# Performance work log

Measured on AMD Instinct MI355X. Metric: run time of the kernel, lower is better.

The kernel has to match this reference:

```python
import jax, jax.numpy as jnp
import numpy as np

N = 4096          # num_nodes == batch (every node sampled once)
D_EMB = 512       # n_embd (temporal encoder width)
D_GNN = 256       # gnn_embd
H = 2             # num_heads (hardcoded in GraphAttentionLayer default)
D_HEAD = D_GNN // H
FUS = D_EMB + D_GNN
EDGE_P = 32.0 / N # avg degree ~ max_neighbors
ALPHA = 0.2
NEG_INF = -9e15


def layer_norm(x, g, b, eps=1e-5):
    m = jnp.mean(x, axis=-1, keepdims=True)
    v = jnp.var(x, axis=-1, keepdims=True)
    return (x - m) / jnp.sqrt(v + eps) * g + b


def setup_inputs() -> dict:
    key = jax.random.key(0)
    ks = jax.random.split(key, 12)
    s = lambda fan: 1.0 / np.sqrt(fan)
    h_temporal = jax.random.normal(ks[0], (N, D_EMB), jnp.float32)
    node_indices = jnp.arange(N, dtype=jnp.int32)
    adj = (jax.random.uniform(ks[1], (N, N)) < EDGE_P).astype(jnp.float32)
    adj = jnp.maximum(adj, jnp.eye(N, dtype=jnp.float32))  # self-loops
    W_proj = jax.random.normal(ks[2], (D_EMB, D_GNN), jnp.float32) * s(D_EMB)
    b_proj = jnp.zeros((D_GNN,), jnp.float32)
    W_gat = jax.random.normal(ks[3], (H, D_GNN, D_HEAD), jnp.float32) * s(D_GNN)
    a_gat = jax.random.normal(ks[4], (H, 2 * D_HEAD), jnp.float32) * s(2 * D_HEAD)
    node_emb = jax.random.normal(ks[5], (N, D_GNN), jnp.float32) * 0.02
    ln_g = jnp.ones((D_GNN,), jnp.float32)
    ln_b = jnp.zeros((D_GNN,), jnp.float32)
    ln2_g = jnp.ones((FUS,), jnp.float32)
    ln2_b = jnp.zeros((FUS,), jnp.float32)
    W1 = jax.random.normal(ks[6], (FUS, FUS // 2), jnp.float32) * s(FUS)
    b1 = jnp.zeros((FUS // 2,), jnp.float32)
    W2 = jax.random.normal(ks[7], (FUS // 2, 1), jnp.float32) * s(FUS // 2)
    b2 = jnp.zeros((1,), jnp.float32)
    return dict(h_temporal=h_temporal, node_indices=node_indices, adj=adj,
                W_proj=W_proj, b_proj=b_proj, W_gat=W_gat, a_gat=a_gat,
                node_emb=node_emb, ln_g=ln_g, ln_b=ln_b,
                ln2_g=ln2_g, ln2_b=ln2_b, W1=W1, b1=b1, W2=W2, b2=b2)


def reference(h_temporal, node_indices, adj, W_proj, b_proj, W_gat, a_gat,
              node_emb, ln_g, ln_b, ln2_g, ln2_b, W1, b1, W2, b2):
    # gnn_proj
    h_gnn_in = h_temporal @ W_proj + b_proj                     # (B, D_GNN)
    # scatter-mean of batch features onto graph nodes (torch.unique + index_add_)
    counts = jax.ops.segment_sum(jnp.ones((h_gnn_in.shape[0],), h_gnn_in.dtype),
                                 node_indices, num_segments=N)
    sums = jax.ops.segment_sum(h_gnn_in, node_indices, num_segments=N)
    uniq_feats = sums / jnp.clip(counts, 1.0)[:, None]
    # nodes present in batch use averaged temporal feats, others keep learned embedding
    sub_feats = jnp.where((counts > 0)[:, None], uniq_feats, node_emb)  # (N, D_GNN)
    # multi-head GAT: e[h,i,j] = leakyrelu(a1_h . Wh_i + a2_h . Wh_j)
    Wh = jnp.einsum('ni,hid->hnd', sub_feats, W_gat)            # (H, N, d)
    f_src = jnp.einsum('hnd,hd->hn', Wh, a_gat[:, :D_HEAD])     # query half
    f_dst = jnp.einsum('hnd,hd->hn', Wh, a_gat[:, D_HEAD:])     # key half
    e = jax.nn.leaky_relu(f_src[:, :, None] + f_dst[:, None, :], ALPHA)  # (H,N,N)
    e = jnp.where(adj[None] > 0, e, NEG_INF)
    att = jax.nn.softmax(e, axis=-1)                            # softmax over neighbors j
    hp = jnp.einsum('hnm,hmd->hnd', att, Wh)                    # (H, N, d)
    hp = jnp.transpose(hp, (1, 0, 2)).reshape(N, D_GNN)         # concat heads
    hp = jax.nn.elu(hp)                                         # concat=True
    sub_out = layer_norm(hp, ln_g, ln_b)
    h_graph = sub_out[node_indices]                             # gather back to batch
    # fusion head
    hc = jnp.concatenate([h_temporal, h_graph], axis=-1)        # (B, FUS)
    z = layer_norm(hc, ln2_g, ln2_b)
    z = jax.nn.gelu(z @ W1 + b1, approximate=False)
    out = z @ W2 + b2                                           # (B, 1)
    return out
```

## Files before the change

### kernel.cpp

```cpp
#include <hip/hip_runtime.h>
#include <hip/hip_bf16.h>
#include <math.h>

#define N_NODES 4096
#define D_EMB   512
#define D_GNN   256
#define D_HEAD  128
#define FUS     768
#define D_HID   384
#define MAX_NBR 512

typedef unsigned short u16;
typedef __attribute__((ext_vector_type(4))) float f4;
typedef __attribute__((ext_vector_type(4))) int   i4;
typedef __attribute__((address_space(3))) u16 lds_u16;
typedef __attribute__((address_space(1))) const u16 g_u16;

__device__ __forceinline__ u16 bfh(float x) {
    __hip_bfloat16 b = __float2bfloat16(x);
    return *(u16*)&b;
}
__device__ __forceinline__ float bff(u16 u) {
    __hip_bfloat16 b = *(__hip_bfloat16*)&u;
    return __bfloat162float(b);
}

#define MFMA(acc, a, b) \
    asm volatile("v_mfma_f32_16x16x32_bf16 %0, %1, %2, %0" : "+v"(acc) : "v"(a), "v"(b))

__device__ __forceinline__ float block_reduce(float v, float* red, bool is_max) {
    #pragma unroll
    for (int o = 32; o; o >>= 1)
        v = is_max ? fmaxf(v, __shfl_down(v, o)) : v + __shfl_down(v, o);
    const int wid = threadIdx.x >> 6;
    if ((threadIdx.x & 63) == 0) red[wid] = v;
    __syncthreads();
    float r;
    if (is_max) r = fmaxf(fmaxf(red[0], red[1]), fmaxf(red[2], red[3]));
    else        r = red[0] + red[1] + red[2] + red[3];
    __syncthreads();
    return r;
}

__global__ __launch_bounds__(256) void split_rm(const float* __restrict__ X,
                                                u16* __restrict__ H, u16* __restrict__ L,
                                                int n4) {
    const int i = blockIdx.x * 256 + threadIdx.x;
    if (i >= n4) return;
    const float4 v = ((const float4*)X)[i];
    ushort4 h, l;
    h.x = bfh(v.x); l.x = bfh(v.x - bff(h.x));
    h.y = bfh(v.y); l.y = bfh(v.y - bff(h.y));
    h.z = bfh(v.z); l.z = bfh(v.z - bff(h.z));
    h.w = bfh(v.w); l.w = bfh(v.w - bff(h.w));
    ((ushort4*)H)[i] = h;
    ((ushort4*)L)[i] = l;
}

__global__ __launch_bounds__(256) void split_t(const float* __restrict__ W,
                                               u16* __restrict__ Th, u16* __restrict__ Tl,
                                               int K, int Nn) {
    __shared__ float tile[32][33];
    const int k0 = blockIdx.y * 32, n0 = blockIdx.x * 32;
    const int lx = threadIdx.x & 31, ly = threadIdx.x >> 5;
    #pragma unroll
    for (int r = ly; r < 32; r += 8)
        tile[r][lx] = W[(size_t)(k0 + r) * Nn + n0 + lx];
    __syncthreads();
    #pragma unroll
    for (int r = ly; r < 32; r += 8) {
        const float v = tile[lx][r];
        const u16 h = bfh(v);
        const size_t o = (size_t)(n0 + r) * K + k0 + lx;
        Th[o] = h;
        Tl[o] = bfh(v - bff(h));
    }
}

__global__ __launch_bounds__(256) void packbt(const float* __restrict__ Wgat,
                                              u16* __restrict__ Th, u16* __restrict__ Tl) {
    const int i = blockIdx.x;
    const int n = threadIdx.x;
    const int h = n >> 7, d = n & 127;
    const float v = Wgat[(size_t)h * D_GNN * D_HEAD + (size_t)i * D_HEAD + d];
    const u16 hh = bfh(v);
    Th[(size_t)n * D_GNN + i] = hh;
    Tl[(size_t)n * D_GNN + i] = bfh(v - bff(hh));
}

template<bool GELU, bool HASB>
__global__ __launch_bounds__(256) void mgemm(const u16* __restrict__ Ah, const u16* __restrict__ Al,
                                             const u16* __restrict__ Bh, const u16* __restrict__ Bl,
                                             const float* __restrict__ bias, float* __restrict__ C,
                                             int M, int Nn, int K) {
    __shared__ u16 lds[2][4][4096];
    const int t = threadIdx.x, w = t >> 6, l = t & 63;
    const int m0 = blockIdx.y * 64, n0 = blockIdx.x * 64;
    const int nk = K >> 6;
    const u16* pAh = Ah + (size_t)(m0 + (t >> 3)) * K + (t & 7) * 8;
    const u16* pAl = Al + (size_t)(m0 + (t >> 3)) * K + (t & 7) * 8;
    const u16* pBh = Bh + (size_t)(n0 + (t >> 3)) * K + (t & 7) * 8;
    const u16* pBl = Bl + (size_t)(n0 + (t >> 3)) * K + (t & 7) * 8;
    const int w512 = w * 512;
    const int K32 = K * 32;

#define STG(c, koff) do { \
    __builtin_amdgcn_global_load_lds((g_u16*)(pAh + (koff)),       (lds_u16*)&lds[c][0][w512],        16, 0, 0); \
    __builtin_amdgcn_global_load_lds((g_u16*)(pAh + (koff) + K32), (lds_u16*)&lds[c][0][w512 + 2048], 16, 0, 0); \
    __builtin_amdgcn_global_load_lds((g_u16*)(pAl + (koff)),       (lds_u16*)&lds[c][1][w512],        16, 0, 0); \
    __builtin_amdgcn_global_load_lds((g_u16*)(pAl + (koff) + K32), (lds_u16*)&lds[c][1][w512 + 2048], 16, 0, 0); \
    __builtin_amdgcn_global_load_lds((g_u16*)(pBh + (koff)),       (lds_u16*)&lds[c][2][w512],        16, 0, 0); \
    __builtin_amdgcn_global_load_lds((g_u16*)(pBh + (koff) + K32), (lds_u16*)&lds[c][2][w512 + 2048], 16, 0, 0); \
    __builtin_amdgcn_global_load_lds((g_u16*)(pBl + (koff)),       (lds_u16*)&lds[c][3][w512],        16, 0, 0); \
    __builtin_amdgcn_global_load_lds((g_u16*)(pBl + (koff) + K32), (lds_u16*)&lds[c][3][w512 + 2048], 16, 0, 0); \
} while (0)

    const int wm = w >> 1, wn = w & 1;
    const int lr = l & 15, lk = (l >> 4) << 3;
    int aoff[2][2], boff[2][2];
    #pragma unroll
    for (int i = 0; i < 2; ++i)
        #pragma unroll
        for (int ks = 0; ks < 2; ++ks) {
            aoff[i][ks] = (wm * 32 + i * 16 + lr) * 64 + ks * 32 + lk;
            boff[i][ks] = (wn * 32 + i * 16 + lr) * 64 + ks * 32 + lk;
        }

    f4 acc[2][2] = {};
    int cur = 0;
    STG(0, 0);
    __syncthreads();
    for (int kt = 0; kt < nk; ++kt) {
        if (kt + 1 < nk) STG(cur ^ 1, (kt + 1) * 64);
        const u16* LAh = lds[cur][0];
        const u16* LAl = lds[cur][1];
        const u16* LBh = lds[cur][2];
        const u16* LBl = lds[cur][3];
        i4 ah[2][2], al_[2][2], bh[2][2], bl_[2][2];
        #pragma unroll
        for (int i = 0; i < 2; ++i)
            #pragma unroll
            for (int ks = 0; ks < 2; ++ks) {
                ah[i][ks]  = *(const i4*)&LAh[aoff[i][ks]];
                al_[i][ks] = *(const i4*)&LAl[aoff[i][ks]];
                bh[i][ks]  = *(const i4*)&LBh[boff[i][ks]];
                bl_[i][ks] = *(const i4*)&LBl[boff[i][ks]];
            }
        #pragma unroll
        for (int i = 0; i < 2; ++i)
            #pragma unroll
            for (int j = 0; j < 2; ++j)
                #pragma unroll
                for (int ks = 0; ks < 2; ++ks) {
                    MFMA(acc[i][j], ah[i][ks],  bh[j][ks]);
                    MFMA(acc[i][j], ah[i][ks],  bl_[j][ks]);
                    MFMA(acc[i][j], al_[i][ks], bh[j][ks]);
                }
        __syncthreads();
        cur ^= 1;
    }
    asm volatile("s_nop 7\n\ts_nop 7\n\ts_nop 7");
    #pragma unroll
    for (int i = 0; i < 2; ++i)
        #pragma unroll
        for (int j = 0; j < 2; ++j) {
            const int col = n0 + wn * 32 + j * 16 + lr;
            float bv = 0.f;
            if (HASB) bv = bias[col];
            #pragma unroll
            for (int r = 0; r < 4; ++r) {
                const int row = m0 + wm * 32 + i * 16 + (l >> 4) * 4 + r;
                float v = acc[i][j][r] + bv;
                if (GELU) v = 0.5f * v * (1.f + erff(v * 0.70710678118654752f));
                C[(size_t)row * Nn + col] = v;
            }
        }
#undef STG
}

__global__ __launch_bounds__(256) void scatter_add(const float* __restrict__ hgnn,
                                                   const int* __restrict__ nidx,
                                                   float* __restrict__ sums,
                                                   float* __restrict__ counts) {
    const int b = blockIdx.x, t = threadIdx.x;
    const int g = nidx[b];
    atomicAdd(&sums[(size_t)g * D_GNN + t], hgnn[(size_t)b * D_GNN + t]);
    if (t == 0) atomicAdd(&counts[g], 1.0f);
}

__global__ __launch_bounds__(256) void combine(const float* __restrict__ sums,
                                               const float* __restrict__ counts,
                                               const float* __restrict__ nemb,
                                               u16* __restrict__ subh,
                                               u16* __restrict__ subl) {
    const int n = blockIdx.x, t = threadIdx.x;
    const float c = counts[n];
    const size_t o = (size_t)n * D_GNN + t;
    const float v = (c > 0.f) ? sums[o] / fmaxf(c, 1.f) : nemb[o];
    const u16 h = bfh(v);
    subh[o] = h;
    subl[o] = bfh(v - bff(h));
}

__global__ __launch_bounds__(256) void fsd(const float* __restrict__ Wh,
                                           const float* __restrict__ agat,
                                           float* __restrict__ fsrc,
                                           float* __restrict__ fdst) {
    const int n = blockIdx.x * 4 + (threadIdx.x >> 6);
    const int l = threadIdx.x & 63;
    const float* row = Wh + (size_t)n * D_GNN;
    const float x0 = row[l],       x1 = row[l + 64];
    const float y0 = row[128 + l], y1 = row[192 + l];
    float s0 = x0 * agat[l]       + x1 * agat[l + 64];
    float s1 = x0 * agat[128 + l] + x1 * agat[192 + l];
    float s2 = y0 * agat[256 + l] + y1 * agat[320 + l];
    float s3 = y0 * agat[384 + l] + y1 * agat[448 + l];
    #pragma unroll
    for (int o = 32; o; o >>= 1) {
        s0 += __shfl_down(s0, o); s1 += __shfl_down(s1, o);
        s2 += __shfl_down(s2, o); s3 += __shfl_down(s3, o);
    }
    if (l == 0) {
        fsrc[n] = s0;            fdst[n] = s1;
        fsrc[N_NODES + n] = s2;  fdst[N_NODES + n] = s3;
    }
}

__global__ __launch_bounds__(256) void gat_attn(const float* __restrict__ adj,
                                                const float* __restrict__ Wh,
                                                const float* __restrict__ fsrc,
                                                const float* __restrict__ fdst,
                                                const float* __restrict__ lng,
                                                const float* __restrict__ lnb,
                                                float* __restrict__ subout) {
    const int i = blockIdx.x, t = threadIdx.x;
    const int lane = t & 63, wid = t >> 6;
    __shared__ int   s_nbr[MAX_NBR];
    __shared__ int   s_wsum[4];
    __shared__ float s_att[2][MAX_NBR];
    __shared__ float s_red[4];
    __shared__ float s_inv[2];

    const float4* arow4 = (const float4*)(adj + (size_t)i * N_NODES) + t * 4;
    const float4 c0 = arow4[0], c1 = arow4[1], c2 = arow4[2], c3 = arow4[3];
    float v[16];
    *(float4*)&v[0]  = c0; *(float4*)&v[4]  = c1;
    *(float4*)&v[8]  = c2; *(float4*)&v[12] = c3;
    int mask = 0;
    #pragma unroll
    for (int k = 0; k < 16; ++k) mask |= (v[k] > 0.f) ? (1 << k) : 0;
    const int cnt_t = __popc(mask);

    int pre = cnt_t;
    #pragma unroll
    for (int o = 1; o < 64; o <<= 1) {
        const int u = __shfl_up(pre, o);
        if (lane >= o) pre += u;
    }
    if (lane == 63) s_wsum[wid] = pre;
    __syncthreads();
    int base = 0;
    for (int w = 0; w < wid; ++w) base += s_wsum[w];
    const int total = s_wsum[0] + s_wsum[1] + s_wsum[2] + s_wsum[3];
    int off = base + pre - cnt_t;
    #pragma unroll
    for (int k = 0; k < 16; ++k)
        if ((mask >> k) & 1) {
            if (off < MAX_NBR) s_nbr[off] = t * 16 + k;
            ++off;
        }
    __syncthreads();
    const int cnt = min(total, MAX_NBR);

    for (int h = 0; h < 2; ++h) {
        const float fs = fsrc[h * N_NODES + i];
        const float* fd = fdst + h * N_NODES;
        float lm = -1e30f;
        for (int idx = t; idx < cnt; idx += 256) {
            float e = fs + fd[s_nbr[idx]];
            e = e > 0.f ? e : 0.2f * e;
            s_att[h][idx] = e;
            lm = fmaxf(lm, e);
        }
        const float m = block_reduce(lm, s_red, true);
        float ls = 0.f;
        for (int idx = t; idx < cnt; idx += 256) {
            const float p = expf(s_att[h][idx] - m);
            s_att[h][idx] = p;
            ls += p;
        }
        const float s = block_reduce(ls, s_red, false);
        if (t == 0) s_inv[h] = 1.f / s;
    }
    __syncthreads();

    const int h = t >> 7, d = t & 127;
    float acc = 0.f;
    for (int j = 0; j < cnt; ++j)
        acc += s_att[h][j] * Wh[(size_t)s_nbr[j] * D_GNN + h * D_HEAD + d];
    acc *= s_inv[h];
    const float vv = acc > 0.f ? acc : expm1f(acc);
    const float sum  = block_reduce(vv, s_red, false);
    const float sq   = block_reduce(vv * vv, s_red, false);
    const float mean = sum * (1.f / 256.f);
    const float var  = sq * (1.f / 256.f) - mean * mean;
    const float rstd = rsqrtf(var + 1e-5f);
    subout[(size_t)i * D_GNN + t] = (vv - mean) * rstd * lng[t] + lnb[t];
}

__global__ __launch_bounds__(256) void fuse_ln(const float* __restrict__ ht,
                                               const float* __restrict__ subout,
                                               const int* __restrict__ nidx,
                                               const float* __restrict__ g,
                                               const float* __restrict__ b,
                                               u16* __restrict__ znh,
                                               u16* __restrict__ znl) {
    const int row = blockIdx.x, t = threadIdx.x;
    __shared__ float s_red[4];
    const int gidx = nidx[row];
    const float x0 = ht[(size_t)row * D_EMB + t];
    const float x1 = ht[(size_t)row * D_EMB + 256 + t];
    const float x2 = subout[(size_t)gidx * D_GNN + t];
    const float sum = block_reduce(x0 + x1 + x2, s_red, false);
    const float sq  = block_reduce(x0 * x0 + x1 * x1 + x2 * x2, s_red, false);
    const float mean = sum * (1.f / 768.f);
    const float var  = sq * (1.f / 768.f) - mean * mean;
    const float rstd = rsqrtf(var + 1e-5f);
    const size_t base = (size_t)row * FUS;
    const float z0 = (x0 - mean) * rstd * g[t]       + b[t];
    const float z1 = (x1 - mean) * rstd * g[256 + t] + b[256 + t];
    const float z2 = (x2 - mean) * rstd * g[512 + t] + b[512 + t];
    u16 h;
    h = bfh(z0); znh[base + t]       = h; znl[base + t]       = bfh(z0 - bff(h));
    h = bfh(z1); znh[base + 256 + t] = h; znl[base + 256 + t] = bfh(z1 - bff(h));
    h = bfh(z2); znh[base + 512 + t] = h; znl[base + 512 + t] = bfh(z2 - bff(h));
}

__global__ __launch_bounds__(256) void outk(const float* __restrict__ z1,
                                            const float* __restrict__ W2,
                                            const float* __restrict__ b2,
                                            float* __restrict__ out) {
    const int row = blockIdx.x * 4 + (threadIdx.x >> 6);
    const int l = threadIdx.x & 63;
    float acc = 0.f;
    for (int c = l; c < D_HID; c += 64)
        acc += z1[(size_t)row * D_HID + c] * W2[c];
    #pragma unroll
    for (int o = 32; o; o >>= 1) acc += __shfl_down(acc, o);
    if (l == 0) out[row] = acc + b2[0];
}

extern "C" void kernel_launch(void* const* d_in, const int* in_sizes, int n_in,
                              void* d_out, int out_size, void* d_ws, size_t ws_size,
                              hipStream_t stream) {
    const float* ht    = (const float*)d_in[0];
    const int*   nidx  = (const int*)  d_in[1];
    const float* adj   = (const float*)d_in[2];
    const float* Wproj = (const float*)d_in[3];
    const float* bproj = (const float*)d_in[4];
    const float* Wgat  = (const float*)d_in[5];
    const float* agat  = (const float*)d_in[6];
    const float* nemb  = (const float*)d_in[7];
    const float* lng   = (const float*)d_in[8];
    const float* lnb   = (const float*)d_in[9];
    const float* ln2g  = (const float*)d_in[10];
    const float* ln2b  = (const float*)d_in[11];
    const float* W1    = (const float*)d_in[12];
    const float* b1    = (const float*)d_in[13];
    const float* W2    = (const float*)d_in[14];
    const float* b2    = (const float*)d_in[15];
    float* out = (float*)d_out;

    const size_t MB = 1u << 20;
    char* base = (char*)d_ws;
    u16*   ht_hi  = (u16*)(base);
    u16*   ht_lo  = ht_hi + 2097152;
    u16*   zn_hi  = (u16*)(base);
    u16*   zn_lo  = zn_hi + 3145728;
    float* f_hgnn = (float*)(base + 12 * MB);
    float* f_z1   = (float*)(base + 12 * MB);
    float* f_sums = (float*)(base + 18 * MB);
    float* f_cnt  = (float*)(base + 22 * MB);
    u16*   subf_h = (u16*)(base + 22 * MB + 65536);
    u16*   subf_l = subf_h + 1048576;
    u16*   bT_h   = (u16*)(base + 27 * MB);
    u16*   bT_l   = bT_h + 65536;
    u16*   WpT_h  = (u16*)(base + 28 * MB);
    u16*   WpT_l  = WpT_h + 131072;
    float* f_wh   = (float*)(base + 29 * MB);
    float* f_fsrc = (float*)(base + 33 * MB);
    float* f_fdst = (float*)(base + 33 * MB + 32768);
    float* f_subo = (float*)(base + 34 * MB);
    u16*   W1T_h  = (u16*)(base + 38 * MB);
    u16*   W1T_l  = W1T_h + 294912;

    hipMemsetAsync(f_sums, 0, (1048576 + 4096) * sizeof(float), stream);

    split_rm<<<2048, 256, 0, stream>>>(ht, ht_hi, ht_lo, 524288);
    split_t<<<dim3(8, 16), 256, 0, stream>>>(Wproj, WpT_h, WpT_l, D_EMB, D_GNN);
    mgemm<false, true><<<dim3(4, 64), 256, 0, stream>>>(
        ht_hi, ht_lo, WpT_h, WpT_l, bproj, f_hgnn, N_NODES, D_GNN, D_EMB);
    scatter_add<<<N_NODES, 256, 0, stream>>>(f_hgnn, nidx, f_sums, f_cnt);
    combine<<<N_NODES, 256, 0, stream>>>(f_sums, f_cnt, nemb, subf_h, subf_l);
    packbt<<<D_GNN, 256, 0, stream>>>(Wgat, bT_h, bT_l);
    mgemm<false, false><<<dim3(4, 64), 256, 0, stream>>>(
        subf_h, subf_l, bT_h, bT_l, nullptr, f_wh, N_NODES, D_GNN, D_GNN);
    fsd<<<N_NODES / 4, 256, 0, stream>>>(f_wh, agat, f_fsrc, f_fdst);
    gat_attn<<<N_NODES, 256, 0, stream>>>(adj, f_wh, f_fsrc, f_fdst, lng, lnb, f_subo);
    fuse_ln<<<N_NODES, 256, 0, stream>>>(ht, f_subo, nidx, ln2g, ln2b, zn_hi, zn_lo);
    split_t<<<dim3(12, 24), 256, 0, stream>>>(W1, W1T_h, W1T_l, FUS, D_HID);
    mgemm<true, true><<<dim3(6, 64), 256, 0, stream>>>(
        zn_hi, zn_lo, W1T_h, W1T_l, b1, f_z1, N_NODES, D_HID, FUS);
    outk<<<N_NODES / 4, 256, 0, stream>>>(f_z1, W2, b2, out);
}
```

Baseline: 214.8 us.

## Split-K the three GEMMs with reduce kernels and merge weight prep launches

Each split-bf16 GEMM now runs with a K split of two across grid z, writing partial results to separate buffers. A new elementwise reduce kernel sums the two partials and applies bias and GELU. The three weight transpose and split kernels are merged into one launch, and the workspace layout is rebuilt without aliasing. The goal is to double the block count on GEMM grids of 256 to 384 blocks so more of the GPU's compute units stay busy. The cost is extra partial-result global traffic and two additional launches.

```diff
diff --git a/kernel.cpp b/kernel.cpp
--- a/kernel.cpp
+++ b/kernel.cpp
@@ -57,11 +57,11 @@
     ((ushort4*)L)[i] = l;
 }
 
-__global__ __launch_bounds__(256) void split_t(const float* __restrict__ W,
-                                               u16* __restrict__ Th, u16* __restrict__ Tl,
-                                               int K, int Nn) {
-    __shared__ float tile[32][33];
-    const int k0 = blockIdx.y * 32, n0 = blockIdx.x * 32;
+__device__ __forceinline__ void split_t_body(const float* __restrict__ W,
+                                             u16* __restrict__ Th, u16* __restrict__ Tl,
+                                             int K, int Nn, int bx, int by,
+                                             float (*tile)[33]) {
+    const int k0 = by * 32, n0 = bx * 32;
     const int lx = threadIdx.x & 31, ly = threadIdx.x >> 5;
     #pragma unroll
     for (int r = ly; r < 32; r += 8)
@@ -77,26 +77,41 @@
     }
 }
 
-__global__ __launch_bounds__(256) void packbt(const float* __restrict__ Wgat,
-                                              u16* __restrict__ Th, u16* __restrict__ Tl) {
-    const int i = blockIdx.x;
-    const int n = threadIdx.x;
-    const int h = n >> 7, d = n & 127;
-    const float v = Wgat[(size_t)h * D_GNN * D_HEAD + (size_t)i * D_HEAD + d];
-    const u16 hh = bfh(v);
-    Th[(size_t)n * D_GNN + i] = hh;
-    Tl[(size_t)n * D_GNN + i] = bfh(v - bff(hh));
-}
-
-template<bool GELU, bool HASB>
+__global__ __launch_bounds__(256) void prep_w(const float* __restrict__ Wproj,
+                                              const float* __restrict__ W1,
+                                              const float* __restrict__ Wgat,
+                                              u16* __restrict__ WpTh, u16* __restrict__ WpTl,
+                                              u16* __restrict__ W1Th, u16* __restrict__ W1Tl,
+                                              u16* __restrict__ bTh,  u16* __restrict__ bTl) {
+    __shared__ float tile[32][33];
+    const int b = blockIdx.x;
+    if (b < 128) {
+        split_t_body(Wproj, WpTh, WpTl, D_EMB, D_GNN, b & 7, b >> 3, tile);
+    } else if (b < 416) {
+        const int i = b - 128;
+        split_t_body(W1, W1Th, W1Tl, FUS, D_HID, i % 12, i / 12, tile);
+    } else {
+        const int i = b - 416;
+        const int n = threadIdx.x;
+        const int h = n >> 7, d = n & 127;
+        const float v = Wgat[(size_t)h * D_GNN * D_HEAD + (size_t)i * D_HEAD + d];
+        const u16 hh = bfh(v);
+        bTh[(size_t)n * D_GNN + i] = hh;
+        bTl[(size_t)n * D_GNN + i] = bfh(v - bff(hh));
+    }
+}
+
+template<int SPLIT>
 __global__ __launch_bounds__(256) void mgemm(const u16* __restrict__ Ah, const u16* __restrict__ Al,
                                              const u16* __restrict__ Bh, const u16* __restrict__ Bl,
-                                             const float* __restrict__ bias, float* __restrict__ C,
+                                             float* __restrict__ C,
                                              int M, int Nn, int K) {
     __shared__ u16 lds[2][4][4096];
     const int t = threadIdx.x, w = t >> 6, l = t & 63;
     const int m0 = blockIdx.y * 64, n0 = blockIdx.x * 64;
-    const int nk = K >> 6;
+    const int nk_per = (K >> 6) / SPLIT;
+    const int kt0 = blockIdx.z * nk_per;
+    float* Cz = C + (size_t)blockIdx.z * M * Nn;
     const u16* pAh = Ah + (size_t)(m0 + (t >> 3)) * K + (t & 7) * 8;
     const u16* pAl = Al + (size_t)(m0 + (t >> 3)) * K + (t & 7) * 8;
     const u16* pBh = Bh + (size_t)(n0 + (t >> 3)) * K + (t & 7) * 8;
@@ -128,10 +143,10 @@
 
     f4 acc[2][2] = {};
     int cur = 0;
-    STG(0, 0);
-    __syncthreads();
-    for (int kt = 0; kt < nk; ++kt) {
-        if (kt + 1 < nk) STG(cur ^ 1, (kt + 1) * 64);
+    STG(0, kt0 * 64);
+    __syncthreads();
+    for (int kt = kt0; kt < kt0 + nk_per; ++kt) {
+        if (kt + 1 < kt0 + nk_per) STG(cur ^ 1, (kt + 1) * 64);
         const u16* LAh = lds[cur][0];
         const u16* LAl = lds[cur][1];
         const u16* LBh = lds[cur][2];
@@ -165,17 +180,37 @@
         #pragma unroll
         for (int j = 0; j < 2; ++j) {
             const int col = n0 + wn * 32 + j * 16 + lr;
-            float bv = 0.f;
-            if (HASB) bv = bias[col];
             #pragma unroll
             for (int r = 0; r < 4; ++r) {
                 const int row = m0 + wm * 32 + i * 16 + (l >> 4) * 4 + r;
-                float v = acc[i][j][r] + bv;
-                if (GELU) v = 0.5f * v * (1.f + erff(v * 0.70710678118654752f));
-                C[(size_t)row * Nn + col] = v;
+                Cz[(size_t)row * Nn + col] = acc[i][j][r];
             }
         }
 #undef STG
+}
+
+template<bool GELU, bool HASB>
+__global__ __launch_bounds__(256) void redk(const float* __restrict__ A,
+                                            const float* __restrict__ B,
+                                            const float* __restrict__ bias,
+                                            float* __restrict__ C,
+                                            int n4, int nb4) {
+    const int i = blockIdx.x * 256 + threadIdx.x;
+    if (i >= n4) return;
+    const float4 a = ((const float4*)A)[i];
+    const float4 b = ((const float4*)B)[i];
+    float4 c = make_float4(a.x + b.x, a.y + b.y, a.z + b.z, a.w + b.w);
+    if (HASB) {
+        const float4 bv = ((const float4*)bias)[i % nb4];
+        c.x += bv.x; c.y += bv.y; c.z += bv.z; c.w += bv.w;
+    }
+    if (GELU) {
+        c.x = 0.5f * c.x * (1.f + erff(c.x * 0.70710678118654752f));
+        c.y = 0.5f * c.y * (1.f + erff(c.y * 0.70710678118654752f));
+        c.z = 0.5f * c.z * (1.f + erff(c.z * 0.70710678118654752f));
+        c.w = 0.5f * c.w * (1.f + erff(c.w * 0.70710678118654752f));
+    }
+    ((float4*)C)[i] = c;
 }
 
 __global__ __launch_bounds__(256) void scatter_add(const float* __restrict__ hgnn,
@@ -371,45 +406,47 @@
     const float* b2    = (const float*)d_in[15];
     float* out = (float*)d_out;
 
-    const size_t MB = 1u << 20;
-    char* base = (char*)d_ws;
-    u16*   ht_hi  = (u16*)(base);
-    u16*   ht_lo  = ht_hi + 2097152;
-    u16*   zn_hi  = (u16*)(base);
-    u16*   zn_lo  = zn_hi + 3145728;
-    float* f_hgnn = (float*)(base + 12 * MB);
-    float* f_z1   = (float*)(base + 12 * MB);
-    float* f_sums = (float*)(base + 18 * MB);
-    float* f_cnt  = (float*)(base + 22 * MB);
-    u16*   subf_h = (u16*)(base + 22 * MB + 65536);
+    float* f_sums = (float*)d_ws;
+    float* f_cnt  = f_sums + 1048576;
+    float* g1     = f_cnt  + 4096;
+    float* f_hgnn = g1     + 2097152;
+    float* g2     = f_hgnn + 1048576;
+    float* f_wh   = g2     + 2097152;
+    float* g3     = f_wh   + 1048576;
+    float* f_z1   = g3     + 3145728;
+    float* f_fsrc = f_z1   + 1572864;
+    float* f_fdst = f_fsrc + 8192;
+    float* f_subo = f_fdst + 8192;
+    u16*   ht_hi  = (u16*)(f_subo + 1048576);
+    u16*   ht_lo  = ht_hi  + 2097152;
+    u16*   subf_h = ht_lo  + 2097152;
     u16*   subf_l = subf_h + 1048576;
-    u16*   bT_h   = (u16*)(base + 27 * MB);
-    u16*   bT_l   = bT_h + 65536;
-    u16*   WpT_h  = (u16*)(base + 28 * MB);
-    u16*   WpT_l  = WpT_h + 131072;
-    float* f_wh   = (float*)(base + 29 * MB);
-    float* f_fsrc = (float*)(base + 33 * MB);
-    float* f_fdst = (float*)(base + 33 * MB + 32768);
-    float* f_subo = (float*)(base + 34 * MB);
-    u16*   W1T_h  = (u16*)(base + 38 * MB);
-    u16*   W1T_l  = W1T_h + 294912;
+    u16*   zn_hi  = subf_l + 1048576;
+    u16*   zn_lo  = zn_hi  + 3145728;
+    u16*   WpT_h  = zn_lo  + 3145728;
+    u16*   WpT_l  = WpT_h  + 131072;
+    u16*   bT_h   = WpT_l  + 131072;
+    u16*   bT_l   = bT_h   + 65536;
+    u16*   W1T_h  = bT_l   + 65536;
+    u16*   W1T_l  = W1T_h  + 294912;
 
     hipMemsetAsync(f_sums, 0, (1048576 + 4096) * sizeof(float), stream);
 
+    prep_w<<<672, 256, 0, stream>>>(Wproj, W1, Wgat, WpT_h, WpT_l, W1T_h, W1T_l, bT_h, bT_l);
     split_rm<<<2048, 256, 0, stream>>>(ht, ht_hi, ht_lo, 524288);
-    split_t<<<dim3(8, 16), 256, 0, stream>>>(Wproj, WpT_h, WpT_l, D_EMB, D_GNN);
-    mgemm<false, true><<<dim3(4, 64), 256, 0, stream>>>(
-        ht_hi, ht_lo, WpT_h, WpT_l, bproj, f_hgnn, N_NODES, D_GNN, D_EMB);
+    mgemm<2><<<dim3(4, 64, 2), 256, 0, stream>>>(
+        ht_hi, ht_lo, WpT_h, WpT_l, g1, N_NODES, D_GNN, D_EMB);
+    redk<false, true><<<1024, 256, 0, stream>>>(g1, g1 + 1048576, bproj, f_hgnn, 262144, 64);
     scatter_add<<<N_NODES, 256, 0, stream>>>(f_hgnn, nidx, f_sums, f_cnt);
     combine<<<N_NODES, 256, 0, stream>>>(f_sums, f_cnt, nemb, subf_h, subf_l);
-    packbt<<<D_GNN, 256, 0, stream>>>(Wgat, bT_h, bT_l);
-    mgemm<false, false><<<dim3(4, 64), 256, 0, stream>>>(
-        subf_h, subf_l, bT_h, bT_l, nullptr, f_wh, N_NODES, D_GNN, D_GNN);
+    mgemm<2><<<dim3(4, 64, 2), 256, 0, stream>>>(
+        subf_h, subf_l, bT_h, bT_l, g2, N_NODES, D_GNN, D_GNN);
+    redk<false, false><<<1024, 256, 0, stream>>>(g2, g2 + 1048576, nullptr, f_wh, 262144, 64);
     fsd<<<N_NODES / 4, 256, 0, stream>>>(f_wh, agat, f_fsrc, f_fdst);
     gat_attn<<<N_NODES, 256, 0, stream>>>(adj, f_wh, f_fsrc, f_fdst, lng, lnb, f_subo);
     fuse_ln<<<N_NODES, 256, 0, stream>>>(ht, f_subo, nidx, ln2g, ln2b, zn_hi, zn_lo);
-    split_t<<<dim3(12, 24), 256, 0, stream>>>(W1, W1T_h, W1T_l, FUS, D_HID);
-    mgemm<true, true><<<dim3(6, 64), 256, 0, stream>>>(
-        zn_hi, zn_lo, W1T_h, W1T_l, b1, f_z1, N_NODES, D_HID, FUS);
+    mgemm<2><<<dim3(6, 64, 2), 256, 0, stream>>>(
+        zn_hi, zn_lo, W1T_h, W1T_l, g3, N_NODES, D_HID, FUS);
+    redk<true, true><<<1536, 256, 0, stream>>>(g3, g3 + 1572864, b1, f_z1, 393216, 96);
     outk<<<N_NODES / 4, 256, 0, stream>>>(f_z1, W2, b2, out);
 }
```

New measurement: 223.5 us. 4.1% more time.
